# Performance work log

Measured on AMD Instinct MI355X. Metric: run time of the kernel, lower is better.

## Reference

```python
import jax, jax.numpy as jnp
import numpy as np

TEMPERATURE = 298.0
SG_HASH = 16  # hashings.atom_hash['CYS']['SG']
COL_BATCH, COL_CHAIN, COL_RESNUM, COL_ATNAME = 0, 1, 2, 3
N_BATCH, N_CHAIN, N_RES = 2, 4, 50000  # static (= runtime max+1 in the torch code)


def setup_inputs() -> dict:
    N, P, A, APR = 500_000, 8_000_000, 4, 10  # atoms, pairs, alternatives, atoms-per-residue
    key = jax.random.key(0)
    ks = jax.random.split(key, 8)
    coords = jax.random.normal(ks[0], (N, 3), dtype=jnp.float32) * 10.0
    at_name = jax.random.randint(ks[1], (N,), 0, 32)
    resnum = jnp.arange(N) // APR  # N_RES = N // APR residues
    batch = jax.random.randint(ks[2], (N,), 0, N_BATCH)
    chain = jax.random.randint(ks[3], (N,), 0, N_CHAIN)
    atom_description = jnp.stack([batch, chain, resnum, at_name], axis=1)
    p0 = jax.random.randint(ks[4], (P,), 0, N)
    off = jax.random.randint(ks[5], (P,), APR, N - APR)  # ensures resnum[p0] != resnum[p1]
    atomPairs = jnp.stack([p0, (p0 + off) % N], axis=1)
    alternativeMask = jax.random.randint(ks[6], (N, A), 0, 2).astype(bool)
    atom_number = jnp.arange(N)
    partners = jnp.zeros((N,), dtype=jnp.int32)
    facc = jax.random.uniform(ks[7], (N,), dtype=jnp.float32)
    return dict(coords=coords, atom_description=atom_description, atom_number=atom_number,
                atomPairs=atomPairs, alternativeMask=alternativeMask, partners=partners, facc=facc)


def reference(coords, atom_description, atom_number, atomPairs, alternativeMask, partners, facc):
    p0, p1 = atomPairs[:, 0], atomPairs[:, 1]
    at_name = atom_description[:, COL_ATNAME]
    sulfur = (at_name[p0] == SG_HASH) & (at_name[p1] == SG_HASH)  # [P] bool; disulfNetwork mask
    # torch.pairwise_distance adds eps=1e-6 to the difference before the norm
    diff = coords[p0] - coords[p1] + 1e-6
    dist = jnp.sqrt(jnp.sum(diff * diff, axis=-1))  # [P]
    resnum = atom_description[:, COL_RESNUM]
    rd = jnp.abs(resnum[p0] - resnum[p1]).astype(jnp.float32)
    safe_rd = jnp.where(sulfur, rd, 1.0)  # keep log finite off the sulfur mask
    energy = -0.001 * TEMPERATURE * (2.1 + 2.9823825 * jnp.log(safe_rd)) + 5.0 * jnp.abs(dist - 2.04)
    netE = jnp.where(sulfur, 0.5 * energy, 0.0)  # masked, halved pair energy [P]
    # bindToAtoms: per-alternative masked scatter-add to both endpoints (vectorized over alts)
    pair_alt = alternativeMask[p0] & alternativeMask[p1]  # [P, A]
    contrib = jnp.where(pair_alt, netE[:, None], 0.0)  # [P, A]
    N, A = alternativeMask.shape
    atomEnergy = jnp.zeros((N, A), jnp.float32).at[p0].add(contrib).at[p1].add(contrib)
    # bindToResi: scatter-add atom energies to (batch, chain, resnum) bins
    flat = (atom_description[:, COL_BATCH] * N_CHAIN + atom_description[:, COL_CHAIN]) * N_RES + resnum
    residueEnergy = jax.ops.segment_sum(atomEnergy, flat, num_segments=N_BATCH * N_CHAIN * N_RES)
    residueEnergy = residueEnergy.reshape(N_BATCH, N_CHAIN, N_RES, A)
    return residueEnergy, atomEnergy, sulfur
```

## Files before the change

kernel.cpp:

```cpp
#include <hip/hip_runtime.h>

#define N_ATOMS   500000
#define N_ALT     4
#define NB        2
#define NC        4
#define NR        50000
#define SG_HASH   16
#define TEMP      298.0f

#define RESE_SIZE  (NB * NC * NR * N_ALT)
#define ATOME_SIZE (N_ATOMS * N_ALT)

#define MASK_W64   ((N_ATOMS + 63) / 64)
#define MASK_W32   (MASK_W64 * 2)

__global__ __launch_bounds__(256) void build_sg_mask(
    const int* __restrict__ adesc,
    unsigned long long* __restrict__ mask)
{
    int i = blockIdx.x * blockDim.x + threadIdx.x;
    bool s = false;
    if (i < N_ATOMS) s = (adesc[(size_t)i * 4 + 3] == SG_HASH);
    unsigned long long b = __ballot(s);
    if ((threadIdx.x & 63) == 0) mask[i >> 6] = b;
}

__device__ __forceinline__ void heavy_pair(
    int p0, int p1,
    const float* __restrict__ coords,
    const int*   __restrict__ adesc,
    const int*   __restrict__ altmask,
    float* __restrict__ resE,
    float* __restrict__ atomE)
{
    int4 d0 = *reinterpret_cast<const int4*>(adesc + (size_t)p0 * 4);
    int4 d1 = *reinterpret_cast<const int4*>(adesc + (size_t)p1 * 4);

    float dx = coords[(size_t)p0 * 3 + 0] - coords[(size_t)p1 * 3 + 0] + 1e-6f;
    float dy = coords[(size_t)p0 * 3 + 1] - coords[(size_t)p1 * 3 + 1] + 1e-6f;
    float dz = coords[(size_t)p0 * 3 + 2] - coords[(size_t)p1 * 3 + 2] + 1e-6f;
    float dist = sqrtf(dx * dx + dy * dy + dz * dz);

    float rd = fabsf((float)(d0.z - d1.z));
    float energy = -0.001f * TEMP * (2.1f + 2.9823825f * logf(rd))
                 + 5.0f * fabsf(dist - 2.04f);
    float netE = 0.5f * energy;

    int4 m0 = *reinterpret_cast<const int4*>(altmask + (size_t)p0 * 4);
    int4 m1 = *reinterpret_cast<const int4*>(altmask + (size_t)p1 * 4);

    int f0 = ((d0.x * NC + d0.y) * NR + d0.z) * N_ALT;
    int f1 = ((d1.x * NC + d1.y) * NR + d1.z) * N_ALT;

    const int* m0p = &m0.x;
    const int* m1p = &m1.x;
#pragma unroll
    for (int a = 0; a < N_ALT; ++a) {
        if (m0p[a] & m1p[a]) {
            atomicAdd(atomE + (size_t)p0 * N_ALT + a, netE);
            atomicAdd(atomE + (size_t)p1 * N_ALT + a, netE);
            atomicAdd(resE + f0 + a, netE);
            atomicAdd(resE + f1 + a, netE);
        }
    }
}

__global__ __launch_bounds__(1024) void disulfide_pair_kernel(
    const float* __restrict__ coords,
    const int*   __restrict__ adesc,
    const int*   __restrict__ pairs,
    const int*   __restrict__ altmask,
    const unsigned int* __restrict__ sgmask32,
    float* __restrict__ resE,
    float* __restrict__ atomE,
    float* __restrict__ sulfur,
    int P)
{
    __shared__ unsigned int lmask[MASK_W32];

    for (int w = threadIdx.x; w < MASK_W32; w += 1024)
        lmask[w] = sgmask32[w];
    __syncthreads();

    const int tid    = blockIdx.x * 1024 + threadIdx.x;
    const int stride = gridDim.x * 1024 * 4;

    for (int i0 = tid * 4; i0 < P; i0 += stride) {
        int4 pa = *reinterpret_cast<const int4*>(pairs + (size_t)i0 * 2);
        int4 pb = *reinterpret_cast<const int4*>(pairs + (size_t)i0 * 2 + 4);

        unsigned m;
        m = (lmask[pa.x >> 5] >> (pa.x & 31)) & (lmask[pa.y >> 5] >> (pa.y & 31));
        bool s0 = m & 1u;
        m = (lmask[pa.z >> 5] >> (pa.z & 31)) & (lmask[pa.w >> 5] >> (pa.w & 31));
        bool s1 = m & 1u;
        m = (lmask[pb.x >> 5] >> (pb.x & 31)) & (lmask[pb.y >> 5] >> (pb.y & 31));
        bool s2 = m & 1u;
        m = (lmask[pb.z >> 5] >> (pb.z & 31)) & (lmask[pb.w >> 5] >> (pb.w & 31));
        bool s3 = m & 1u;

        float4 sv = make_float4(s0 ? 1.0f : 0.0f, s1 ? 1.0f : 0.0f,
                                s2 ? 1.0f : 0.0f, s3 ? 1.0f : 0.0f);
        *reinterpret_cast<float4*>(sulfur + i0) = sv;

        if (s0) heavy_pair(pa.x, pa.y, coords, adesc, altmask, resE, atomE);
        if (s1) heavy_pair(pa.z, pa.w, coords, adesc, altmask, resE, atomE);
        if (s2) heavy_pair(pb.x, pb.y, coords, adesc, altmask, resE, atomE);
        if (s3) heavy_pair(pb.z, pb.w, coords, adesc, altmask, resE, atomE);
    }
}

extern "C" void kernel_launch(void* const* d_in, const int* in_sizes, int n_in,
                              void* d_out, int out_size, void* d_ws, size_t ws_size,
                              hipStream_t stream) {
    const float* coords  = (const float*)d_in[0];
    const int*   adesc   = (const int*)d_in[1];
    const int*   pairs   = (const int*)d_in[3];
    const int*   altmask = (const int*)d_in[4];

    const int P = in_sizes[3] / 2;

    float* out    = (float*)d_out;
    float* resE   = out;
    float* atomE  = out + RESE_SIZE;
    float* sulfur = out + RESE_SIZE + ATOME_SIZE;

    unsigned long long* sgmask = (unsigned long long*)d_ws;

    hipMemsetAsync(d_out, 0, (size_t)(RESE_SIZE + ATOME_SIZE) * sizeof(float), stream);

    {
        const int threads = 256;
        const int blocks  = (N_ATOMS + threads - 1) / threads;
        build_sg_mask<<<blocks, threads, 0, stream>>>(adesc, sgmask);
    }

    {
        const int threads = 1024;
        const int blocks  = 512;
        disulfide_pair_kernel<<<blocks, threads, 0, stream>>>(
            coords, adesc, pairs, altmask, (const unsigned int*)sgmask,
            resE, atomE, sulfur, P);
    }
}
```

Measured before the change: 32.60 us.

## Fuse output zeroing into mask kernel, process 8 pairs per thread with nontemporal IO

Replaces the separate hipMemsetAsync with zeroing done inside the SG-mask build kernel, which saves one launch/command. The pair kernel now handles 8 pairs per thread per iteration instead of 4. It uses nontemporal loads for pair indices and nontemporal stores for the sulfur flags, so this streaming data is less likely to pollute cache. The trade-off is a larger prep grid and more registers per thread in the main kernel.

```diff
diff --git a/kernel.cpp b/kernel.cpp
--- a/kernel.cpp
+++ b/kernel.cpp
@@ -10,19 +10,30 @@
 
 #define RESE_SIZE  (NB * NC * NR * N_ALT)
 #define ATOME_SIZE (N_ATOMS * N_ALT)
+#define ZERO_F4    ((RESE_SIZE + ATOME_SIZE) / 4)
 
 #define MASK_W64   ((N_ATOMS + 63) / 64)
 #define MASK_W32   (MASK_W64 * 2)
 
-__global__ __launch_bounds__(256) void build_sg_mask(
+typedef int   intx4 __attribute__((ext_vector_type(4)));
+typedef float fltx4 __attribute__((ext_vector_type(4)));
+
+__global__ __launch_bounds__(1024) void prep_kernel(
     const int* __restrict__ adesc,
+    float* __restrict__ zero_base,
     unsigned long long* __restrict__ mask)
 {
-    int i = blockIdx.x * blockDim.x + threadIdx.x;
+    int i = blockIdx.x * 1024 + threadIdx.x;
+
+    if (i < ZERO_F4) {
+        fltx4 z = {0.f, 0.f, 0.f, 0.f};
+        reinterpret_cast<fltx4*>(zero_base)[i] = z;
+    }
+
     bool s = false;
     if (i < N_ATOMS) s = (adesc[(size_t)i * 4 + 3] == SG_HASH);
     unsigned long long b = __ballot(s);
-    if ((threadIdx.x & 63) == 0) mask[i >> 6] = b;
+    if (i < N_ATOMS && (threadIdx.x & 63) == 0) mask[i >> 6] = b;
 }
 
 __device__ __forceinline__ void heavy_pair(
@@ -65,6 +76,12 @@
     }
 }
 
+__device__ __forceinline__ bool probe2(const unsigned int* __restrict__ lm,
+                                       int a, int b) {
+    unsigned m = (lm[a >> 5] >> (a & 31)) & (lm[b >> 5] >> (b & 31));
+    return m & 1u;
+}
+
 __global__ __launch_bounds__(1024) void disulfide_pair_kernel(
     const float* __restrict__ coords,
     const int*   __restrict__ adesc,
@@ -83,30 +100,40 @@
     __syncthreads();
 
     const int tid    = blockIdx.x * 1024 + threadIdx.x;
-    const int stride = gridDim.x * 1024 * 4;
+    const int stride = gridDim.x * 1024 * 8;
 
-    for (int i0 = tid * 4; i0 < P; i0 += stride) {
-        int4 pa = *reinterpret_cast<const int4*>(pairs + (size_t)i0 * 2);
-        int4 pb = *reinterpret_cast<const int4*>(pairs + (size_t)i0 * 2 + 4);
+    for (int i0 = tid * 8; i0 < P; i0 += stride) {
+        const intx4* pp = reinterpret_cast<const intx4*>(pairs + (size_t)i0 * 2);
+        intx4 pa = __builtin_nontemporal_load(pp + 0);
+        intx4 pb = __builtin_nontemporal_load(pp + 1);
+        intx4 pc = __builtin_nontemporal_load(pp + 2);
+        intx4 pd = __builtin_nontemporal_load(pp + 3);
 
-        unsigned m;
-        m = (lmask[pa.x >> 5] >> (pa.x & 31)) & (lmask[pa.y >> 5] >> (pa.y & 31));
-        bool s0 = m & 1u;
-        m = (lmask[pa.z >> 5] >> (pa.z & 31)) & (lmask[pa.w >> 5] >> (pa.w & 31));
-        bool s1 = m & 1u;
-        m = (lmask[pb.x >> 5] >> (pb.x & 31)) & (lmask[pb.y >> 5] >> (pb.y & 31));
-        bool s2 = m & 1u;
-        m = (lmask[pb.z >> 5] >> (pb.z & 31)) & (lmask[pb.w >> 5] >> (pb.w & 31));
-        bool s3 = m & 1u;
+        bool s0 = probe2(lmask, pa.x, pa.y);
+        bool s1 = probe2(lmask, pa.z, pa.w);
+        bool s2 = probe2(lmask, pb.x, pb.y);
+        bool s3 = probe2(lmask, pb.z, pb.w);
+        bool s4 = probe2(lmask, pc.x, pc.y);
+        bool s5 = probe2(lmask, pc.z, pc.w);
+        bool s6 = probe2(lmask, pd.x, pd.y);
+        bool s7 = probe2(lmask, pd.z, pd.w);
 
-        float4 sv = make_float4(s0 ? 1.0f : 0.0f, s1 ? 1.0f : 0.0f,
-                                s2 ? 1.0f : 0.0f, s3 ? 1.0f : 0.0f);
-        *reinterpret_cast<float4*>(sulfur + i0) = sv;
+        fltx4 sv0 = {s0 ? 1.0f : 0.0f, s1 ? 1.0f : 0.0f,
+                     s2 ? 1.0f : 0.0f, s3 ? 1.0f : 0.0f};
+        fltx4 sv1 = {s4 ? 1.0f : 0.0f, s5 ? 1.0f : 0.0f,
+                     s6 ? 1.0f : 0.0f, s7 ? 1.0f : 0.0f};
+        fltx4* sp = reinterpret_cast<fltx4*>(sulfur + i0);
+        __builtin_nontemporal_store(sv0, sp + 0);
+        __builtin_nontemporal_store(sv1, sp + 1);
 
         if (s0) heavy_pair(pa.x, pa.y, coords, adesc, altmask, resE, atomE);
         if (s1) heavy_pair(pa.z, pa.w, coords, adesc, altmask, resE, atomE);
         if (s2) heavy_pair(pb.x, pb.y, coords, adesc, altmask, resE, atomE);
         if (s3) heavy_pair(pb.z, pb.w, coords, adesc, altmask, resE, atomE);
+        if (s4) heavy_pair(pc.x, pc.y, coords, adesc, altmask, resE, atomE);
+        if (s5) heavy_pair(pc.z, pc.w, coords, adesc, altmask, resE, atomE);
+        if (s6) heavy_pair(pd.x, pd.y, coords, adesc, altmask, resE, atomE);
+        if (s7) heavy_pair(pd.z, pd.w, coords, adesc, altmask, resE, atomE);
     }
 }
 
@@ -127,12 +154,10 @@
 
     unsigned long long* sgmask = (unsigned long long*)d_ws;
 
-    hipMemsetAsync(d_out, 0, (size_t)(RESE_SIZE + ATOME_SIZE) * sizeof(float), stream);
-
     {
-        const int threads = 256;
-        const int blocks  = (N_ATOMS + threads - 1) / threads;
-        build_sg_mask<<<blocks, threads, 0, stream>>>(adesc, sgmask);
+        const int threads = 1024;
+        const int blocks  = (ZERO_F4 + threads - 1) / threads;
+        prep_kernel<<<blocks, threads, 0, stream>>>(adesc, resE, sgmask);
     }
 
     {
```

Result: slower. 42.25 us (+29.6%).
